# Kernel tuning notes

Measured on AMD Instinct MI355X. Metric: run time of the kernel, lower is better.

## Reference

```python
import jax, jax.numpy as jnp
import numpy as np

SEQ, D, H, DFF, L, MAXINT = 8, 2, 2, 32, 2, 255
V = MAXINT + 1
BATCH = 131072


def _layer_norm(x, g, b, eps=1e-5):
    mu = jnp.mean(x, axis=-1, keepdims=True)
    var = jnp.mean((x - mu) ** 2, axis=-1, keepdims=True)
    return (x - mu) / jnp.sqrt(var + eps) * g + b


def setup_inputs() -> dict:
    key = jax.random.key(0)
    ks = jax.random.split(key, 8)
    f = lambda k, shape: (jax.random.normal(k, shape, dtype=jnp.float32) * 0.2)
    x = jax.random.randint(ks[0], (BATCH, SEQ), 0, 256)
    return {
        "x": x,
        "Wqkv": f(ks[1], (L, 3 * D, D)), "bqkv": jnp.zeros((L, 3 * D), jnp.float32),
        "Wo": f(ks[2], (L, D, D)), "bo": jnp.zeros((L, D), jnp.float32),
        "W1": f(ks[3], (L, DFF, D)), "b1": jnp.zeros((L, DFF), jnp.float32),
        "W2": f(ks[4], (L, D, DFF)), "b2": jnp.zeros((L, D), jnp.float32),
        "g1": jnp.ones((L, D), jnp.float32), "be1": jnp.zeros((L, D), jnp.float32),
        "g2": jnp.ones((L, D), jnp.float32), "be2": jnp.zeros((L, D), jnp.float32),
        "Wout": f(ks[5], (V, D)), "bout": jnp.zeros((V,), jnp.float32),
    }


def reference(x, Wqkv, bqkv, Wo, bo, W1, b1, W2, b2, g1, be1, g2, be2, Wout, bout):
    B, S = x.shape
    hd = D // H                      # head_dim = 1
    scale = 1.0 / np.sqrt(hd)
    numbers = x.astype(jnp.float32) / MAXINT
    positions = jnp.broadcast_to(jnp.arange(S, dtype=jnp.float32) / (S - 1), (B, S))
    h = jnp.stack([numbers, positions], axis=-1)  # [B, S, D]

    for l in range(L):  # small fixed layer count
        qkv = h @ Wqkv[l].T + bqkv[l]             # [B, S, 3D]
        q, k, v = jnp.split(qkv, 3, axis=-1)
        sh = lambda t: t.reshape(B, S, H, hd).transpose(0, 2, 1, 3)  # [B,H,S,hd]
        q, k, v = sh(q), sh(k), sh(v)
        scores = jnp.einsum('bhqd,bhkd->bhqk', q, k) * scale
        attn = jax.nn.softmax(scores, axis=-1)
        o = jnp.einsum('bhqk,bhkd->bhqd', attn, v)
        o = o.transpose(0, 2, 1, 3).reshape(B, S, D) @ Wo[l].T + bo[l]
        h = _layer_norm(h + o, g1[l], be1[l])      # post-norm (norm_first=False)
        ff = jax.nn.gelu(h @ W1[l].T + b1[l], approximate=False) @ W2[l].T + b2[l]
        h = _layer_norm(h + ff, g2[l], be2[l])

    final = h[:, -1]                               # [B, D]
    return final @ Wout.T + bout                   # [B, V]
```

## Files before the change

kernel.cpp:

```cpp
#include <hip/hip_runtime.h>
#include <math.h>

#define SEQ   8
#define DFF   32
#define NL    2
#define VOCAB 256
#define BATCH 131072
#define TBL_N 256

__global__ __launch_bounds__(256) void build_tables_par(
    const float* __restrict__ W1, const float* __restrict__ b1,
    const float* __restrict__ W2, const float* __restrict__ b2,
    const float* __restrict__ g1, const float* __restrict__ be1,
    float4* __restrict__ T4)
{
    int gt    = blockIdx.x * 256 + threadIdx.x;
    int entry = gt >> 5;
    int j     = gt & 31;
    if (entry >= NL * TBL_N) return;
    int l = entry >> 8;
    int i = entry & (TBL_N - 1);

    float nd0 = -1.0f + (float)i * (2.0f / TBL_N);
    float nd1 = nd0 + (2.0f / TBL_N);

    float ga = g1[l*2+0], gb = g1[l*2+1], ba = be1[l*2+0], bb = be1[l*2+1];
    float w1a = W1[l*64 + j*2], w1b = W1[l*64 + j*2 + 1], b1j = b1[l*32 + j];
    float w2a = W2[l*64 + j],   w2b = W2[l*64 + 32 + j];

    float h0 = fmaf( nd0, ga, ba), h1 = fmaf(-nd0, gb, bb);
    float t  = fmaf(w1a, h0, fmaf(w1b, h1, b1j));
    float g  = 0.5f * t * (1.0f + erff(t * 0.70710678118654752f));
    float f00 = g * w2a, f10 = g * w2b;
    h0 = fmaf( nd1, ga, ba); h1 = fmaf(-nd1, gb, bb);
    t  = fmaf(w1a, h0, fmaf(w1b, h1, b1j));
    g  = 0.5f * t * (1.0f + erff(t * 0.70710678118654752f));
    float f01 = g * w2a, f11 = g * w2b;

    #pragma unroll
    for (int m = 1; m < 32; m <<= 1) {
        f00 += __shfl_xor(f00, m, 32);
        f10 += __shfl_xor(f10, m, 32);
        f01 += __shfl_xor(f01, m, 32);
        f11 += __shfl_xor(f11, m, 32);
    }
    if (j == 0) {
        T4[entry] = make_float4(f00 + b2[l*2+0], f10 + b2[l*2+1],
                                f01 + b2[l*2+0], f11 + b2[l*2+1]);
    }
}

__global__ __launch_bounds__(256, 8) void seqtx_main(
    const int*   __restrict__ x,
    const float* __restrict__ Wqkv, const float* __restrict__ bqkv,
    const float* __restrict__ Wo,   const float* __restrict__ bo,
    const float* __restrict__ g1,   const float* __restrict__ be1,
    const float* __restrict__ g2,   const float* __restrict__ be2,
    const float* __restrict__ Wout, const float* __restrict__ bout,
    const float4* __restrict__ T4,
    float* __restrict__ out)
{
    __shared__ float4 tbl[NL * TBL_N];
    __shared__ float4 exch[256];

    const int tid   = threadIdx.x;
    const int sub   = tid & 7;
    const int gid   = blockIdx.x * 256 + tid;
    const int lane  = tid & 63;
    const int g8    = (tid >> 3) & 7;
    const int gbase = tid & ~7;

    tbl[tid]       = T4[tid];
    tbl[tid + 256] = T4[tid + 256];

    const int cg = lane * 4;
    const float2* wvp = reinterpret_cast<const float2*>(Wout);
    float2 wv0 = wvp[cg + 0];
    float2 wv1 = wvp[cg + 1];
    float2 wv2 = wvp[cg + 2];
    float2 wv3 = wvp[cg + 3];
    float4 bv  = *reinterpret_cast<const float4*>(bout + cg);

    float h0 = (float)x[gid] * (1.0f / 255.0f);
    float h1 = (float)sub * (1.0f / 7.0f);

    __syncthreads();

    float ndl;

    {
        const float* wq = Wqkv;
        const float* bq = bqkv;
        float q0 = fmaf(wq[0],  h0, fmaf(wq[1],  h1, bq[0]));
        float q1 = fmaf(wq[2],  h0, fmaf(wq[3],  h1, bq[1]));
        float k0 = fmaf(wq[4],  h0, fmaf(wq[5],  h1, bq[2]));
        float k1 = fmaf(wq[6],  h0, fmaf(wq[7],  h1, bq[3]));
        float v0 = fmaf(wq[8],  h0, fmaf(wq[9],  h1, bq[4]));
        float v1 = fmaf(wq[10], h0, fmaf(wq[11], h1, bq[5]));

        exch[gbase | ((sub + g8) & 7)] = make_float4(k0, v0, k1, v1);
        __builtin_amdgcn_wave_barrier();

        float q0e = q0 * 1.44269504f;
        float q1e = q1 * 1.44269504f;
        float s0 = 0.0f, a0 = 0.0f, s1 = 0.0f, a1 = 0.0f;
        #pragma unroll
        for (int j = 0; j < SEQ; ++j) {
            float4 kv = exch[gbase | ((j + g8) & 7)];
            float e0 = __builtin_amdgcn_exp2f(q0e * kv.x);
            s0 += e0;  a0 = fmaf(e0, kv.y, a0);
            float e1 = __builtin_amdgcn_exp2f(q1e * kv.z);
            s1 += e1;  a1 = fmaf(e1, kv.w, a1);
        }
        float o0 = a0 * __builtin_amdgcn_rcpf(s0);
        float o1 = a1 * __builtin_amdgcn_rcpf(s1);

        float p0 = fmaf(Wo[0], o0, fmaf(Wo[1], o1, bo[0]));
        float p1 = fmaf(Wo[2], o0, fmaf(Wo[3], o1, bo[1]));
        float a = h0 + p0, c = h1 + p1;
        float d = 0.5f * (a - c);
        float nd = d * __builtin_amdgcn_rsqf(fmaf(d, d, 1e-5f));
        h0 = fmaf( nd, g1[0], be1[0]);
        h1 = fmaf(-nd, g1[1], be1[1]);

        float tf = fmaf(nd, (float)(TBL_N / 2), (float)(TBL_N / 2));
        int   i  = (int)tf;
        i = (i < 0) ? 0 : ((i > TBL_N - 1) ? TBL_N - 1 : i);
        float fr = tf - (float)i;
        float4 e4 = tbl[i];
        float f0 = fmaf(fr, e4.z - e4.x, e4.x);
        float f1 = fmaf(fr, e4.w - e4.y, e4.y);

        a = h0 + f0;  c = h1 + f1;
        d = 0.5f * (a - c);
        float nd2 = d * __builtin_amdgcn_rsqf(fmaf(d, d, 1e-5f));
        h0 = fmaf( nd2, g2[0], be2[0]);
        h1 = fmaf(-nd2, g2[1], be2[1]);
    }

    {
        const float* wq = Wqkv + 12;
        const float* bq = bqkv + 6;
        float q0 = fmaf(wq[0],  h0, fmaf(wq[1],  h1, bq[0]));
        float q1 = fmaf(wq[2],  h0, fmaf(wq[3],  h1, bq[1]));
        float k0 = fmaf(wq[4],  h0, fmaf(wq[5],  h1, bq[2]));
        float k1 = fmaf(wq[6],  h0, fmaf(wq[7],  h1, bq[3]));
        float v0 = fmaf(wq[8],  h0, fmaf(wq[9],  h1, bq[4]));
        float v1 = fmaf(wq[10], h0, fmaf(wq[11], h1, bq[5]));

        float q0e = __shfl(q0, 7, SEQ) * 1.44269504f;
        float q1e = __shfl(q1, 7, SEQ) * 1.44269504f;
        float e0 = __builtin_amdgcn_exp2f(q0e * k0);
        float e1 = __builtin_amdgcn_exp2f(q1e * k1);
        float n0 = e0 * v0, n1 = e1 * v1;
        #pragma unroll
        for (int m = 1; m < SEQ; m <<= 1) {
            e0 += __shfl_xor(e0, m, SEQ);
            n0 += __shfl_xor(n0, m, SEQ);
            e1 += __shfl_xor(e1, m, SEQ);
            n1 += __shfl_xor(n1, m, SEQ);
        }
        float o0 = n0 * __builtin_amdgcn_rcpf(e0);
        float o1 = n1 * __builtin_amdgcn_rcpf(e1);

        float p0 = fmaf(Wo[4], o0, fmaf(Wo[5], o1, bo[2]));
        float p1 = fmaf(Wo[6], o0, fmaf(Wo[7], o1, bo[3]));
        float a = h0 + p0, c = h1 + p1;
        float d = 0.5f * (a - c);
        float nd = d * __builtin_amdgcn_rsqf(fmaf(d, d, 1e-5f));
        float hh0 = fmaf( nd, g1[2], be1[2]);
        float hh1 = fmaf(-nd, g1[3], be1[3]);

        float tf = fmaf(nd, (float)(TBL_N / 2), (float)(TBL_N / 2));
        int   i  = (int)tf;
        i = (i < 0) ? 0 : ((i > TBL_N - 1) ? TBL_N - 1 : i);
        float fr = tf - (float)i;
        float4 e4 = tbl[TBL_N + i];
        float f0 = fmaf(fr, e4.z - e4.x, e4.x);
        float f1 = fmaf(fr, e4.w - e4.y, e4.y);

        a = hh0 + f0;  c = hh1 + f1;
        d = 0.5f * (a - c);
        ndl = d * __builtin_amdgcn_rsqf(fmaf(d, d, 1e-5f));
    }

    float gf0 = g2[2], gf1 = g2[3], bf0 = be2[2], bf1 = be2[3];
    float u0 = wv0.x * gf0 - wv0.y * gf1,  w0 = fmaf(wv0.x, bf0, fmaf(wv0.y, bf1, bv.x));
    float u1 = wv1.x * gf0 - wv1.y * gf1,  w1 = fmaf(wv1.x, bf0, fmaf(wv1.y, bf1, bv.y));
    float u2 = wv2.x * gf0 - wv2.y * gf1,  w2 = fmaf(wv2.x, bf0, fmaf(wv2.y, bf1, bv.z));
    float u3 = wv3.x * gf0 - wv3.y * gf1,  w3 = fmaf(wv3.x, bf0, fmaf(wv3.y, bf1, bv.w));

    const size_t rowbase = (size_t)(gid >> 6) * 8;
    #pragma unroll
    for (int e = 0; e < 8; ++e) {
        float ndv = __int_as_float(
            __builtin_amdgcn_readlane(__float_as_int(ndl), e * 8 + 7));
        float4 res;
        res.x = fmaf(ndv, u0, w0);
        res.y = fmaf(ndv, u1, w1);
        res.z = fmaf(ndv, u2, w2);
        res.w = fmaf(ndv, u3, w3);
        *reinterpret_cast<float4*>(&out[(rowbase + e) * VOCAB + cg]) = res;
    }
}

extern "C" void kernel_launch(void* const* d_in, const int* in_sizes, int n_in,
                              void* d_out, int out_size, void* d_ws, size_t ws_size,
                              hipStream_t stream) {
    const int*   x    = (const int*)  d_in[0];
    const float* Wqkv = (const float*)d_in[1];
    const float* bqkv = (const float*)d_in[2];
    const float* Wo   = (const float*)d_in[3];
    const float* bo   = (const float*)d_in[4];
    const float* W1   = (const float*)d_in[5];
    const float* b1   = (const float*)d_in[6];
    const float* W2   = (const float*)d_in[7];
    const float* b2   = (const float*)d_in[8];
    const float* g1   = (const float*)d_in[9];
    const float* be1  = (const float*)d_in[10];
    const float* g2   = (const float*)d_in[11];
    const float* be2  = (const float*)d_in[12];
    const float* Wout = (const float*)d_in[13];
    const float* bout = (const float*)d_in[14];
    float* out = (float*)d_out;

    float4* T4 = (float4*)d_ws;

    build_tables_par<<<(NL * TBL_N * 32) / 256, 256, 0, stream>>>(
        W1, b1, W2, b2, g1, be1, T4);

    seqtx_main<<<BATCH / 32, 256, 0, stream>>>(
        x, Wqkv, bqkv, Wo, bo, g1, be1, g2, be2, Wout, bout, T4, out);
}
```

Measured before the change: 33.75 us.

## Drop FFN lookup table; compute GELU FFN inline in a single kernel

Removes the separate table-building kernel and the shared-memory interpolation table, and instead evaluates the 32-wide GELU feed-forward directly in the main kernel, using an Abramowitz-Stegun erf approximation. In layer 2 only the last position is needed, so the FFN is split across the 8 lanes of each sequence group and reduced with shuffles, with the residual taken from lane 7. This removes a kernel launch, the table load and the block barrier. In exchange it adds per-thread transcendental and FMA work in layer 1 (32 GELUs per token) and changes numerics from table interpolation to a polynomial erf.

```diff
diff --git a/kernel.cpp b/kernel.cpp
--- a/kernel.cpp
+++ b/kernel.cpp
@@ -6,61 +6,31 @@
 #define NL    2
 #define VOCAB 256
 #define BATCH 131072
-#define TBL_N 256
-
-__global__ __launch_bounds__(256) void build_tables_par(
-    const float* __restrict__ W1, const float* __restrict__ b1,
-    const float* __restrict__ W2, const float* __restrict__ b2,
-    const float* __restrict__ g1, const float* __restrict__ be1,
-    float4* __restrict__ T4)
-{
-    int gt    = blockIdx.x * 256 + threadIdx.x;
-    int entry = gt >> 5;
-    int j     = gt & 31;
-    if (entry >= NL * TBL_N) return;
-    int l = entry >> 8;
-    int i = entry & (TBL_N - 1);
-
-    float nd0 = -1.0f + (float)i * (2.0f / TBL_N);
-    float nd1 = nd0 + (2.0f / TBL_N);
-
-    float ga = g1[l*2+0], gb = g1[l*2+1], ba = be1[l*2+0], bb = be1[l*2+1];
-    float w1a = W1[l*64 + j*2], w1b = W1[l*64 + j*2 + 1], b1j = b1[l*32 + j];
-    float w2a = W2[l*64 + j],   w2b = W2[l*64 + 32 + j];
-
-    float h0 = fmaf( nd0, ga, ba), h1 = fmaf(-nd0, gb, bb);
-    float t  = fmaf(w1a, h0, fmaf(w1b, h1, b1j));
-    float g  = 0.5f * t * (1.0f + erff(t * 0.70710678118654752f));
-    float f00 = g * w2a, f10 = g * w2b;
-    h0 = fmaf( nd1, ga, ba); h1 = fmaf(-nd1, gb, bb);
-    t  = fmaf(w1a, h0, fmaf(w1b, h1, b1j));
-    g  = 0.5f * t * (1.0f + erff(t * 0.70710678118654752f));
-    float f01 = g * w2a, f11 = g * w2b;
-
-    #pragma unroll
-    for (int m = 1; m < 32; m <<= 1) {
-        f00 += __shfl_xor(f00, m, 32);
-        f10 += __shfl_xor(f10, m, 32);
-        f01 += __shfl_xor(f01, m, 32);
-        f11 += __shfl_xor(f11, m, 32);
-    }
-    if (j == 0) {
-        T4[entry] = make_float4(f00 + b2[l*2+0], f10 + b2[l*2+1],
-                                f01 + b2[l*2+0], f11 + b2[l*2+1]);
-    }
+
+__device__ __forceinline__ float gelu_f(float t) {
+    float ax = fabsf(t);
+    float k  = __builtin_amdgcn_rcpf(fmaf(0.3275911f, ax, 1.0f));
+    float p  = fmaf(k, 1.061405429f, -1.453152027f);
+    p = fmaf(k, p, 1.421413741f);
+    p = fmaf(k, p, -0.284496736f);
+    p = fmaf(k, p, 0.254829592f);
+    p = p * k;
+    float e  = __builtin_amdgcn_exp2f(-1.44269504f * ax * ax);
+    float er = copysignf(fmaf(-p, e, 1.0f), t);
+    return 0.5f * t * (1.0f + er);
 }
 
-__global__ __launch_bounds__(256, 8) void seqtx_main(
+__global__ __launch_bounds__(256, 8) void seqtx_one(
     const int*   __restrict__ x,
     const float* __restrict__ Wqkv, const float* __restrict__ bqkv,
     const float* __restrict__ Wo,   const float* __restrict__ bo,
+    const float* __restrict__ W1,   const float* __restrict__ b1,
+    const float* __restrict__ W2,   const float* __restrict__ b2,
     const float* __restrict__ g1,   const float* __restrict__ be1,
     const float* __restrict__ g2,   const float* __restrict__ be2,
     const float* __restrict__ Wout, const float* __restrict__ bout,
-    const float4* __restrict__ T4,
     float* __restrict__ out)
 {
-    __shared__ float4 tbl[NL * TBL_N];
     __shared__ float4 exch[256];
 
     const int tid   = threadIdx.x;
@@ -69,9 +39,6 @@
     const int lane  = tid & 63;
     const int g8    = (tid >> 3) & 7;
     const int gbase = tid & ~7;
-
-    tbl[tid]       = T4[tid];
-    tbl[tid + 256] = T4[tid + 256];
 
     const int cg = lane * 4;
     const float2* wvp = reinterpret_cast<const float2*>(Wout);
@@ -83,8 +50,6 @@
 
     float h0 = (float)x[gid] * (1.0f / 255.0f);
     float h1 = (float)sub * (1.0f / 7.0f);
-
-    __syncthreads();
 
     float ndl;
 
@@ -123,13 +88,13 @@
         h0 = fmaf( nd, g1[0], be1[0]);
         h1 = fmaf(-nd, g1[1], be1[1]);
 
-        float tf = fmaf(nd, (float)(TBL_N / 2), (float)(TBL_N / 2));
-        int   i  = (int)tf;
-        i = (i < 0) ? 0 : ((i > TBL_N - 1) ? TBL_N - 1 : i);
-        float fr = tf - (float)i;
-        float4 e4 = tbl[i];
-        float f0 = fmaf(fr, e4.z - e4.x, e4.x);
-        float f1 = fmaf(fr, e4.w - e4.y, e4.y);
+        float f0 = b2[0], f1 = b2[1];
+        for (int j = 0; j < DFF; ++j) {
+            float t = fmaf(W1[j * 2], h0, fmaf(W1[j * 2 + 1], h1, b1[j]));
+            float g = gelu_f(t);
+            f0 = fmaf(g, W2[j], f0);
+            f1 = fmaf(g, W2[32 + j], f1);
+        }
 
         a = h0 + f0;  c = h1 + f1;
         d = 0.5f * (a - c);
@@ -163,21 +128,32 @@
         float o0 = n0 * __builtin_amdgcn_rcpf(e0);
         float o1 = n1 * __builtin_amdgcn_rcpf(e1);
 
+        float hp0 = __shfl(h0, 7, SEQ);
+        float hp1 = __shfl(h1, 7, SEQ);
         float p0 = fmaf(Wo[4], o0, fmaf(Wo[5], o1, bo[2]));
         float p1 = fmaf(Wo[6], o0, fmaf(Wo[7], o1, bo[3]));
-        float a = h0 + p0, c = h1 + p1;
+        float a = hp0 + p0, c = hp1 + p1;
         float d = 0.5f * (a - c);
         float nd = d * __builtin_amdgcn_rsqf(fmaf(d, d, 1e-5f));
         float hh0 = fmaf( nd, g1[2], be1[2]);
         float hh1 = fmaf(-nd, g1[3], be1[3]);
 
-        float tf = fmaf(nd, (float)(TBL_N / 2), (float)(TBL_N / 2));
-        int   i  = (int)tf;
-        i = (i < 0) ? 0 : ((i > TBL_N - 1) ? TBL_N - 1 : i);
-        float fr = tf - (float)i;
-        float4 e4 = tbl[TBL_N + i];
-        float f0 = fmaf(fr, e4.z - e4.x, e4.x);
-        float f1 = fmaf(fr, e4.w - e4.y, e4.y);
+        float f0p = 0.0f, f1p = 0.0f;
+        #pragma unroll
+        for (int m = 0; m < 4; ++m) {
+            int j = sub + m * 8;
+            float t = fmaf(W1[64 + j * 2], hh0, fmaf(W1[64 + j * 2 + 1], hh1, b1[32 + j]));
+            float g = gelu_f(t);
+            f0p = fmaf(g, W2[64 + j], f0p);
+            f1p = fmaf(g, W2[96 + j], f1p);
+        }
+        #pragma unroll
+        for (int m = 1; m < SEQ; m <<= 1) {
+            f0p += __shfl_xor(f0p, m, SEQ);
+            f1p += __shfl_xor(f1p, m, SEQ);
+        }
+        float f0 = f0p + b2[2];
+        float f1 = f1p + b2[3];
 
         a = hh0 + f0;  c = hh1 + f1;
         d = 0.5f * (a - c);
@@ -224,11 +200,6 @@
     const float* bout = (const float*)d_in[14];
     float* out = (float*)d_out;
 
-    float4* T4 = (float4*)d_ws;
-
-    build_tables_par<<<(NL * TBL_N * 32) / 256, 256, 0, stream>>>(
-        W1, b1, W2, b2, g1, be1, T4);
-
-    seqtx_main<<<BATCH / 32, 256, 0, stream>>>(
-        x, Wqkv, bqkv, Wo, bo, g1, be1, g2, be2, Wout, bout, T4, out);
+    seqtx_one<<<BATCH / 32, 256, 0, stream>>>(
+        x, Wqkv, bqkv, Wo, bo, W1, b1, W2, b2, g1, be1, g2, be2, Wout, bout, out);
 }
```

Result: no change. 34.04 us (+0.9%).
